# Performance work log

Measured on AMD Instinct MI355X. Metric: run time of the kernel, lower is better.

Reference implementation:

```python
import jax, jax.numpy as jnp
import numpy as np

DEPTH = 8
INPUT_WIDTH = 64
INNER_WIDTH = 32
BATCH = 65536
N_NODES = 2 ** DEPTH - 1   # 255 inner nodes
N_LEAVES = 2 ** DEPTH      # 256 bins
EPS = 1e-8


def _tree_paths(depth):
    """For each leaf, the inner-node index at each level and whether the path
    goes right (right child uses 1 - decision, mirroring hstack([p, 1-p]) indexing)."""
    node_idx = np.zeros((2 ** depth, depth), dtype=np.int32)
    is_right = np.zeros((2 ** depth, depth), dtype=bool)
    for leaf in range(2 ** depth):
        idx = 0
        for level in range(depth):
            bit = (leaf >> (depth - 1 - level)) & 1
            node_idx[leaf, level] = idx
            is_right[leaf, level] = bool(bit)
            idx = 2 * idx + 1 + bit
    return node_idx, is_right

_NODE_IDX_NP, _IS_RIGHT_NP = _tree_paths(DEPTH)
NODE_IDX = jnp.asarray(_NODE_IDX_NP)   # [L, depth]
IS_RIGHT = jnp.asarray(_IS_RIGHT_NP)   # [L, depth]


def _init_b_i():
    """Replicates PartialRadialLayer.init_tree_weights: thresholds evenly dividing [0,1],
    stored as logits so sigmoid(b_i) recovers the threshold."""
    b = np.zeros(N_NODES, dtype=np.float64)
    b[0] = -0.5
    used = 1
    for i in range(1, DEPTH):
        n_nodes = 2 ** i
        div = float(2 ** (i + 1))
        for node in range(n_nodes):
            b[used + node] = -(2 * node + 1) / div
        used += n_nodes
    return np.log(-b / (1.0 + b)).astype(np.float32).reshape(1, -1)


def setup_inputs() -> dict:
    key = jax.random.key(0)
    kx, kr, kt = jax.random.split(key, 3)
    x = jax.random.normal(kx, (BATCH, INPUT_WIDTH), dtype=jnp.float32)
    # kaiming_normal_ on [1, input_width]: fan_in = input_width
    ray = jax.random.normal(kr, (1, INPUT_WIDTH), dtype=jnp.float32) * np.sqrt(2.0 / INPUT_WIDTH)
    # kaiming_normal_ on [L, I, W]: fan_in = I * W
    inner_transforms = jax.random.normal(kt, (N_LEAVES, INPUT_WIDTH, INNER_WIDTH), dtype=jnp.float32) * np.sqrt(2.0 / (INPUT_WIDTH * INNER_WIDTH))
    w_i = jnp.zeros((1, N_NODES), dtype=jnp.float32)
    a_i = 5.0 * jnp.ones((1, N_NODES), dtype=jnp.float32)
    b_i = jnp.asarray(_init_b_i())
    return {"x": x, "ray": ray, "inner_transforms": inner_transforms,
            "w_i": w_i, "b_i": b_i, "a_i": a_i}


def reference(x, ray, inner_transforms, w_i, b_i, a_i):
    # angles: arccos(cosine_similarity(x, ray)) / pi
    x_norm = jnp.maximum(jnp.linalg.norm(x, axis=1), EPS)            # [B]
    r_norm = jnp.maximum(jnp.linalg.norm(ray, axis=1), EPS)          # [1]
    cos = jnp.clip((x @ ray[0]) / (x_norm * r_norm), -1.0, 1.0)      # [B]
    angles = jnp.arccos(cos) / jnp.pi                                # [B]

    # per-node decisions
    node_fns = (0.5 + jax.nn.sigmoid(w_i)) * angles[:, None] - jax.nn.sigmoid(b_i)  # [B, N]
    decisions = jax.nn.sigmoid(node_fns * (1.0 + a_i))                               # [B, N]

    # soft bin distribution: product along each root-to-leaf path
    g = decisions[:, NODE_IDX]                       # [B, L, depth]
    vals = jnp.where(IS_RIGHT, 1.0 - g, g)           # right child -> 1 - p
    distribution = jnp.prod(vals, axis=2)            # [B, L]

    # weighted per-leaf transforms: einsum('bi,liw->blw') then ('bl,blo->bo'), fused
    out = jnp.einsum('bl,bi,liw->bw', distribution, x, inner_transforms)
    return out
```

## Files before the change

### kernel.cpp

```cpp
#include <hip/hip_runtime.h>
#include <hip/hip_bf16.h>

#define NLEAF 256
#define MBLK 256
#define THREADS 512

typedef __attribute__((ext_vector_type(4))) float f32x4;
typedef __attribute__((ext_vector_type(4))) unsigned int uint4v;
typedef __attribute__((ext_vector_type(8))) __bf16 bf16x8;
typedef __attribute__((ext_vector_type(4))) __bf16 bf16x4;

#define OFF_DIST 0
#define OFF_XP   131072
#define OFF_AC   147456
#define OFF_BC   148480
#define OFF_ANG  149504
#define OFF_RAY  150528
#define SMEM_BYTES 150784

__device__ __forceinline__ float sigf(float s) { return 1.0f / (1.0f + __expf(-s)); }

__device__ __forceinline__ int permr(int r) {
  return (r & 0xC3) | ((r & 0x30) >> 2) | ((r & 0x0C) << 2);
}

__global__ __launch_bounds__(256) void prep_T(const float* __restrict__ T,
                                              __bf16* __restrict__ wsT) {
  __shared__ char tile[4096];
  const int l = blockIdx.x;
  const float* src = T + (size_t)l * 2048;
  const int t = threadIdx.x;
#pragma unroll
  for (int p = 0; p < 2; ++p) {
    int e = p * 1024 + t * 4;
    f32x4 v = *(const f32x4*)(src + e);
    int k = e >> 5, w0 = e & 31;
#pragma unroll
    for (int j = 0; j < 4; ++j) {
      int w = w0 + j;
      int off = (w * 128 + 2 * k) ^ ((w & 7) << 4);
      *(__bf16*)(tile + off) = (__bf16)v[j];
    }
  }
  __syncthreads();
  *(uint4v*)((char*)wsT + (size_t)l * 4096 + t * 16) = *(const uint4v*)(tile + t * 16);
}

template <bool USE_WS>
__global__ __launch_bounds__(THREADS, 2)
void prl_main(const float* __restrict__ x, const float* __restrict__ ray,
              const float* __restrict__ w_i, const float* __restrict__ b_i,
              const float* __restrict__ a_i, const void* __restrict__ tsrc,
              float* __restrict__ out) {
  extern __shared__ char smem[];
  const int tid = threadIdx.x;
  const int lane = tid & 63;
  const int wid = tid >> 6;
  const int rg = wid >> 1;
  const int cg = wid & 1;
  const int g = lane >> 4;
  const int ln = lane & 15;
  const int row0 = blockIdx.x * MBLK;

  float* A_c = (float*)(smem + OFF_AC);
  float* B_c = (float*)(smem + OFF_BC);
  float* angles = (float*)(smem + OFF_ANG);
  float* ray_l = (float*)(smem + OFF_RAY);
  __bf16* distb = (__bf16*)(smem + OFF_DIST);

  if (tid < 255) {
    float aa = 1.0f + a_i[tid];
    A_c[tid] = (0.5f + sigf(w_i[tid])) * aa;
    B_c[tid] = -sigf(b_i[tid]) * aa;
  }
  if (tid >= 256 && tid < 320) ray_l[tid - 256] = ray[tid - 256];
  __syncthreads();

  bf16x8 afrag[4][2] = {};
  float* xp = (float*)(smem + OFF_XP);
  for (int c = 0; c < 4; ++c) {
    const float* xg = x + (size_t)(row0 + c * 64) * 64;
#pragma unroll
    for (int p = 0; p < 2; ++p) {
      int idx = p * 512 + tid;
      f32x4 v = *(const f32x4*)(xg + idx * 4);
      *(f32x4*)(xp + idx * 4) = v;
      int cgr = idx & 15;
      f32x4 rv = *(const f32x4*)(ray_l + cgr * 4);
      float a0 = v[0] * v[0] + v[1] * v[1] + v[2] * v[2] + v[3] * v[3];
      float a1 = v[0] * rv[0] + v[1] * rv[1] + v[2] * rv[2] + v[3] * rv[3];
      float a2 = rv[0] * rv[0] + rv[1] * rv[1] + rv[2] * rv[2] + rv[3] * rv[3];
#pragma unroll
      for (int s = 1; s < 16; s <<= 1) {
        a0 += __shfl_xor(a0, s, 64);
        a1 += __shfl_xor(a1, s, 64);
        a2 += __shfl_xor(a2, s, 64);
      }
      if ((tid & 15) == 0) {
        int r = idx >> 4;
        float xn = fmaxf(sqrtf(a0), 1e-8f);
        float rn = fmaxf(sqrtf(a2), 1e-8f);
        float cs = a1 / (xn * rn);
        cs = fminf(fmaxf(cs, -1.0f), 1.0f);
        angles[c * 64 + r] = acosf(cs) * 0.31830988618379067f;
      }
    }
    __syncthreads();
    if (rg == c) {
#pragma unroll
      for (int mt = 0; mt < 4; ++mt)
#pragma unroll
        for (int kt = 0; kt < 2; ++kt) {
          int rl = mt * 16 + ln;
          int k0 = kt * 32 + g * 8;
          f32x4 u0 = *(const f32x4*)(xp + rl * 64 + k0);
          f32x4 u1 = *(const f32x4*)(xp + rl * 64 + k0 + 4);
          bf16x8 af;
          af[0] = (__bf16)u0[0]; af[1] = (__bf16)u0[1];
          af[2] = (__bf16)u0[2]; af[3] = (__bf16)u0[3];
          af[4] = (__bf16)u1[0]; af[5] = (__bf16)u1[1];
          af[6] = (__bf16)u1[2]; af[7] = (__bf16)u1[3];
          afrag[mt][kt] = af;
        }
    }
    __syncthreads();
  }

  __bf16* PA = (__bf16*)(smem + OFF_XP);
  __bf16* PB = (__bf16*)(smem + OFF_XP + 8192);
  if (tid < 256) {
    float ang = angles[tid];
    float d = sigf(fmaf(A_c[0], ang, B_c[0]));
    PA[tid] = (__bf16)d;
    PA[256 + tid] = (__bf16)(1.0f - d);
  }
  __syncthreads();
  {
    int n = tid >> 8, r = tid & 255;
    float p = (float)PA[tid];
    float ang = angles[r];
    float d = sigf(fmaf(A_c[1 + n], ang, B_c[1 + n]));
    PB[(2 * n) * 256 + r] = (__bf16)(p * d);
    PB[(2 * n + 1) * 256 + r] = (__bf16)(p * (1.0f - d));
  }
  __syncthreads();
#pragma unroll
  for (int it = 0; it < 2; ++it) {
    int e = it * 512 + tid;
    int n = e >> 8, r = e & 255;
    float p = (float)PB[e];
    float ang = angles[r];
    float d = sigf(fmaf(A_c[3 + n], ang, B_c[3 + n]));
    PA[(2 * n) * 256 + r] = (__bf16)(p * d);
    PA[(2 * n + 1) * 256 + r] = (__bf16)(p * (1.0f - d));
  }
  __syncthreads();
#pragma unroll
  for (int it = 0; it < 4; ++it) {
    int e = it * 512 + tid;
    int n = e >> 8, r = e & 255;
    float p = (float)PA[e];
    float ang = angles[r];
    float d = sigf(fmaf(A_c[7 + n], ang, B_c[7 + n]));
    PB[(2 * n) * 256 + r] = (__bf16)(p * d);
    PB[(2 * n + 1) * 256 + r] = (__bf16)(p * (1.0f - d));
  }
  __syncthreads();
  {
    const int r = tid & 255;
    const int pr = permr(r);
    const float ang = angles[r];
#pragma unroll
    for (int it = 0; it < 8; ++it) {
      int n4 = it * 2 + (tid >> 8);
      float p4 = (float)PB[n4 * 256 + r];
      float d4 = sigf(fmaf(A_c[15 + n4], ang, B_c[15 + n4]));
      float p5[2] = {p4 * d4, p4 * (1.0f - d4)};
#pragma unroll
      for (int b5 = 0; b5 < 2; ++b5) {
        int n5 = 2 * n4 + b5;
        float d5 = sigf(fmaf(A_c[31 + n5], ang, B_c[31 + n5]));
        float p6[2] = {p5[b5] * d5, p5[b5] * (1.0f - d5)};
#pragma unroll
        for (int b6 = 0; b6 < 2; ++b6) {
          int n6 = 2 * n5 + b6;
          float d6 = sigf(fmaf(A_c[63 + n6], ang, B_c[63 + n6]));
          float p7[2] = {p6[b6] * d6, p6[b6] * (1.0f - d6)};
#pragma unroll
          for (int b7 = 0; b7 < 2; ++b7) {
            int n7 = 2 * n6 + b7;
            float d7 = sigf(fmaf(A_c[127 + n7], ang, B_c[127 + n7]));
            float pv = p7[b7];
            distb[(2 * n7) * 256 + pr] = (__bf16)(pv * d7);
            distb[(2 * n7 + 1) * 256 + pr] = (__bf16)(pv * (1.0f - d7));
          }
        }
      }
    }
  }
  __syncthreads();

  f32x4 acc[4] = {};
  const int wB = cg * 16 + ln;
  const int ad0 = (wB * 128 + g * 16) ^ ((wB & 7) << 4);
  const int ad1 = (wB * 128 + 64 + g * 16) ^ ((wB & 7) << 4);

  auto compute = [&](bf16x8 bk0, bf16x8 bk1, int l) {
    const __bf16* dp = distb + l * 256 + rg * 64 + g * 16;
    bf16x8 q0 = *(const bf16x8*)dp;
    bf16x8 q1 = *(const bf16x8*)(dp + 8);
    f32x4 dv[4];
    dv[0] = (f32x4){(float)q0[0], (float)q0[1], (float)q0[2], (float)q0[3]};
    dv[1] = (f32x4){(float)q0[4], (float)q0[5], (float)q0[6], (float)q0[7]};
    dv[2] = (f32x4){(float)q1[0], (float)q1[1], (float)q1[2], (float)q1[3]};
    dv[3] = (f32x4){(float)q1[4], (float)q1[5], (float)q1[6], (float)q1[7]};
    f32x4 zero = {0.0f, 0.0f, 0.0f, 0.0f};
#pragma unroll
    for (int mt = 0; mt < 4; ++mt) {
      f32x4 y = __builtin_amdgcn_mfma_f32_16x16x32_bf16(afrag[mt][0], bk0, zero, 0, 0, 0);
      y = __builtin_amdgcn_mfma_f32_16x16x32_bf16(afrag[mt][1], bk1, y, 0, 0, 0);
      acc[mt] += dv[mt] * y;
    }
  };

  char* tb = smem + OFF_XP;

  if constexpr (USE_WS) {
    const int ts = tid >> 8;
    const int to = (tid & 255) * 16;
    uint4v tv = *(const uint4v*)((const char*)tsrc + ts * 4096 + to);
    *(uint4v*)(tb + ts * 4096 + to) = tv;
    tv = *(const uint4v*)((const char*)tsrc + (2 + ts) * 4096 + to);
    __syncthreads();
    for (int l = 0; l < NLEAF; l += 2) {
      char* cur = tb + ((l >> 1) & 1) * 8192;
      char* nxt = tb + (((l >> 1) + 1) & 1) * 8192;
      if (l + 2 < NLEAF) {
        *(uint4v*)(nxt + ts * 4096 + to) = tv;
        if (l + 4 < NLEAF)
          tv = *(const uint4v*)((const char*)tsrc + (size_t)(l + 4 + ts) * 4096 + to);
      }
      compute(*(const bf16x8*)(cur + ad0), *(const bf16x8*)(cur + ad1), l);
      compute(*(const bf16x8*)(cur + 4096 + ad0), *(const bf16x8*)(cur + 4096 + ad1), l + 1);
      __syncthreads();
    }
  } else {
    for (int l = 0; l < NLEAF; ++l) {
      const float* tp0 = (const float*)tsrc + (size_t)l * 2048 + (g * 8) * 32 + wB;
      const float* tp1 = tp0 + 32 * 32;
      bf16x8 bk0, bk1;
#pragma unroll
      for (int j = 0; j < 8; ++j) {
        bk0[j] = (__bf16)tp0[j * 32];
        bk1[j] = (__bf16)tp1[j * 32];
      }
      compute(bk0, bk1, l);
    }
  }

#pragma unroll
  for (int mt = 0; mt < 4; ++mt)
#pragma unroll
    for (int e = 0; e < 4; ++e) {
      int row = row0 + rg * 64 + mt * 16 + g * 4 + e;
      out[(size_t)row * 32 + cg * 16 + ln] = acc[mt][e];
    }
}

extern "C" void kernel_launch(void* const* d_in, const int* in_sizes, int n_in,
                              void* d_out, int out_size, void* d_ws, size_t ws_size,
                              hipStream_t stream) {
  const float* x = (const float*)d_in[0];
  const float* ray = (const float*)d_in[1];
  const float* T = (const float*)d_in[2];
  const float* w_i = (const float*)d_in[3];
  const float* b_i = (const float*)d_in[4];
  const float* a_i = (const float*)d_in[5];
  float* out = (float*)d_out;

  bool use_ws = ws_size >= (size_t)NLEAF * 4096;
  if (use_ws) {
    hipFuncSetAttribute(reinterpret_cast<const void*>(&prl_main<true>),
                        hipFuncAttributeMaxDynamicSharedMemorySize, SMEM_BYTES);
    prep_T<<<256, 256, 0, stream>>>(T, (__bf16*)d_ws);
    prl_main<true><<<256, THREADS, SMEM_BYTES, stream>>>(x, ray, w_i, b_i, a_i, d_ws, out);
  } else {
    hipFuncSetAttribute(reinterpret_cast<const void*>(&prl_main<false>),
                        hipFuncAttributeMaxDynamicSharedMemorySize, SMEM_BYTES);
    prl_main<false><<<256, THREADS, SMEM_BYTES, stream>>>(x, ray, w_i, b_i, a_i, T, out);
  }
}
```

Baseline: 174.6 us.

## Halve rows per block to double grid size and fit more blocks per CU

Each block now handles 128 rows instead of 256, so the grid has 512 blocks instead of 256. Shared memory is roughly halved and the launch bound now asks for 4 blocks per SM, both aimed at raising occupancy and filling all CUs. The leaf loop now stages one leaf of the transform per iteration instead of two, which means a barrier on every leaf. Each block also reloads the full bf16 transform set, so total transform traffic from L2 doubles.

Result: faster. 165.3 us (-5.3%).

```diff
diff --git a/kernel.cpp b/kernel.cpp
--- a/kernel.cpp
+++ b/kernel.cpp
@@ -2,7 +2,7 @@
 #include <hip/hip_bf16.h>
 
 #define NLEAF 256
-#define MBLK 256
+#define MBLK 128
 #define THREADS 512
 
 typedef __attribute__((ext_vector_type(4))) float f32x4;
@@ -11,17 +11,17 @@
 typedef __attribute__((ext_vector_type(4))) __bf16 bf16x4;
 
 #define OFF_DIST 0
-#define OFF_XP   131072
-#define OFF_AC   147456
-#define OFF_BC   148480
-#define OFF_ANG  149504
-#define OFF_RAY  150528
-#define SMEM_BYTES 150784
+#define OFF_T    65536
+#define OFF_AC   73728
+#define OFF_BC   74752
+#define OFF_ANG  75776
+#define OFF_RAY  76288
+#define SMEM_BYTES 76544
 
 __device__ __forceinline__ float sigf(float s) { return 1.0f / (1.0f + __expf(-s)); }
 
 __device__ __forceinline__ int permr(int r) {
-  return (r & 0xC3) | ((r & 0x30) >> 2) | ((r & 0x0C) << 2);
+  return (r & 0x63) | ((r & 0x0C) << 1) | ((r & 0x10) >> 2);
 }
 
 __global__ __launch_bounds__(256) void prep_T(const float* __restrict__ T,
@@ -47,7 +47,7 @@
 }
 
 template <bool USE_WS>
-__global__ __launch_bounds__(THREADS, 2)
+__global__ __launch_bounds__(THREADS, 4)
 void prl_main(const float* __restrict__ x, const float* __restrict__ ray,
               const float* __restrict__ w_i, const float* __restrict__ b_i,
               const float* __restrict__ a_i, const void* __restrict__ tsrc,
@@ -76,12 +76,11 @@
   if (tid >= 256 && tid < 320) ray_l[tid - 256] = ray[tid - 256];
   __syncthreads();
 
-  bf16x8 afrag[4][2] = {};
-  float* xp = (float*)(smem + OFF_XP);
-  for (int c = 0; c < 4; ++c) {
-    const float* xg = x + (size_t)(row0 + c * 64) * 64;
-#pragma unroll
-    for (int p = 0; p < 2; ++p) {
+  float* xp = (float*)(smem + OFF_DIST);
+  {
+    const float* xg = x + (size_t)row0 * 64;
+#pragma unroll
+    for (int p = 0; p < 4; ++p) {
       int idx = p * 512 + tid;
       f32x4 v = *(const f32x4*)(xg + idx * 4);
       *(f32x4*)(xp + idx * 4) = v;
@@ -102,78 +101,76 @@
         float rn = fmaxf(sqrtf(a2), 1e-8f);
         float cs = a1 / (xn * rn);
         cs = fminf(fmaxf(cs, -1.0f), 1.0f);
-        angles[c * 64 + r] = acosf(cs) * 0.31830988618379067f;
-      }
-    }
-    __syncthreads();
-    if (rg == c) {
-#pragma unroll
-      for (int mt = 0; mt < 4; ++mt)
-#pragma unroll
-        for (int kt = 0; kt < 2; ++kt) {
-          int rl = mt * 16 + ln;
-          int k0 = kt * 32 + g * 8;
-          f32x4 u0 = *(const f32x4*)(xp + rl * 64 + k0);
-          f32x4 u1 = *(const f32x4*)(xp + rl * 64 + k0 + 4);
-          bf16x8 af;
-          af[0] = (__bf16)u0[0]; af[1] = (__bf16)u0[1];
-          af[2] = (__bf16)u0[2]; af[3] = (__bf16)u0[3];
-          af[4] = (__bf16)u1[0]; af[5] = (__bf16)u1[1];
-          af[6] = (__bf16)u1[2]; af[7] = (__bf16)u1[3];
-          afrag[mt][kt] = af;
-        }
-    }
-    __syncthreads();
-  }
-
-  __bf16* PA = (__bf16*)(smem + OFF_XP);
-  __bf16* PB = (__bf16*)(smem + OFF_XP + 8192);
-  if (tid < 256) {
+        angles[r] = acosf(cs) * 0.31830988618379067f;
+      }
+    }
+  }
+  __syncthreads();
+
+  bf16x8 afrag[2][2];
+#pragma unroll
+  for (int mt = 0; mt < 2; ++mt)
+#pragma unroll
+    for (int kt = 0; kt < 2; ++kt) {
+      int rl = rg * 32 + mt * 16 + ln;
+      int k0 = kt * 32 + g * 8;
+      f32x4 u0 = *(const f32x4*)(xp + rl * 64 + k0);
+      f32x4 u1 = *(const f32x4*)(xp + rl * 64 + k0 + 4);
+      bf16x8 af;
+      af[0] = (__bf16)u0[0]; af[1] = (__bf16)u0[1];
+      af[2] = (__bf16)u0[2]; af[3] = (__bf16)u0[3];
+      af[4] = (__bf16)u1[0]; af[5] = (__bf16)u1[1];
+      af[6] = (__bf16)u1[2]; af[7] = (__bf16)u1[3];
+      afrag[mt][kt] = af;
+    }
+  __syncthreads();
+
+  __bf16* PA = (__bf16*)(smem + OFF_T);
+  __bf16* PB = (__bf16*)(smem + OFF_T + 4096);
+  if (tid < 128) {
     float ang = angles[tid];
     float d = sigf(fmaf(A_c[0], ang, B_c[0]));
     PA[tid] = (__bf16)d;
-    PA[256 + tid] = (__bf16)(1.0f - d);
-  }
-  __syncthreads();
-  {
-    int n = tid >> 8, r = tid & 255;
+    PA[128 + tid] = (__bf16)(1.0f - d);
+  }
+  __syncthreads();
+  if (tid < 256) {
+    int n = tid >> 7, r = tid & 127;
     float p = (float)PA[tid];
     float ang = angles[r];
     float d = sigf(fmaf(A_c[1 + n], ang, B_c[1 + n]));
-    PB[(2 * n) * 256 + r] = (__bf16)(p * d);
-    PB[(2 * n + 1) * 256 + r] = (__bf16)(p * (1.0f - d));
+    PB[(2 * n) * 128 + r] = (__bf16)(p * d);
+    PB[(2 * n + 1) * 128 + r] = (__bf16)(p * (1.0f - d));
+  }
+  __syncthreads();
+  {
+    int n = tid >> 7, r = tid & 127;
+    float p = (float)PB[tid];
+    float ang = angles[r];
+    float d = sigf(fmaf(A_c[3 + n], ang, B_c[3 + n]));
+    PA[(2 * n) * 128 + r] = (__bf16)(p * d);
+    PA[(2 * n + 1) * 128 + r] = (__bf16)(p * (1.0f - d));
   }
   __syncthreads();
 #pragma unroll
   for (int it = 0; it < 2; ++it) {
     int e = it * 512 + tid;
-    int n = e >> 8, r = e & 255;
-    float p = (float)PB[e];
-    float ang = angles[r];
-    float d = sigf(fmaf(A_c[3 + n], ang, B_c[3 + n]));
-    PA[(2 * n) * 256 + r] = (__bf16)(p * d);
-    PA[(2 * n + 1) * 256 + r] = (__bf16)(p * (1.0f - d));
-  }
-  __syncthreads();
-#pragma unroll
-  for (int it = 0; it < 4; ++it) {
-    int e = it * 512 + tid;
-    int n = e >> 8, r = e & 255;
+    int n = e >> 7, r = e & 127;
     float p = (float)PA[e];
     float ang = angles[r];
     float d = sigf(fmaf(A_c[7 + n], ang, B_c[7 + n]));
-    PB[(2 * n) * 256 + r] = (__bf16)(p * d);
-    PB[(2 * n + 1) * 256 + r] = (__bf16)(p * (1.0f - d));
+    PB[(2 * n) * 128 + r] = (__bf16)(p * d);
+    PB[(2 * n + 1) * 128 + r] = (__bf16)(p * (1.0f - d));
   }
   __syncthreads();
   {
-    const int r = tid & 255;
+    const int r = tid & 127;
     const int pr = permr(r);
     const float ang = angles[r];
 #pragma unroll
-    for (int it = 0; it < 8; ++it) {
-      int n4 = it * 2 + (tid >> 8);
-      float p4 = (float)PB[n4 * 256 + r];
+    for (int it = 0; it < 4; ++it) {
+      int n4 = it * 4 + (tid >> 7);
+      float p4 = (float)PB[n4 * 128 + r];
       float d4 = sigf(fmaf(A_c[15 + n4], ang, B_c[15 + n4]));
       float p5[2] = {p4 * d4, p4 * (1.0f - d4)};
 #pragma unroll
@@ -191,80 +188,77 @@
             int n7 = 2 * n6 + b7;
             float d7 = sigf(fmaf(A_c[127 + n7], ang, B_c[127 + n7]));
             float pv = p7[b7];
-            distb[(2 * n7) * 256 + pr] = (__bf16)(pv * d7);
-            distb[(2 * n7 + 1) * 256 + pr] = (__bf16)(pv * (1.0f - d7));
+            distb[(2 * n7) * 128 + pr] = (__bf16)(pv * d7);
+            distb[(2 * n7 + 1) * 128 + pr] = (__bf16)(pv * (1.0f - d7));
           }
         }
       }
     }
   }
-  __syncthreads();
-
-  f32x4 acc[4] = {};
+
+  f32x4 acc0 = {}, acc1 = {};
   const int wB = cg * 16 + ln;
   const int ad0 = (wB * 128 + g * 16) ^ ((wB & 7) << 4);
   const int ad1 = (wB * 128 + 64 + g * 16) ^ ((wB & 7) << 4);
-
-  auto compute = [&](bf16x8 bk0, bf16x8 bk1, int l) {
-    const __bf16* dp = distb + l * 256 + rg * 64 + g * 16;
-    bf16x8 q0 = *(const bf16x8*)dp;
-    bf16x8 q1 = *(const bf16x8*)(dp + 8);
-    f32x4 dv[4];
-    dv[0] = (f32x4){(float)q0[0], (float)q0[1], (float)q0[2], (float)q0[3]};
-    dv[1] = (f32x4){(float)q0[4], (float)q0[5], (float)q0[6], (float)q0[7]};
-    dv[2] = (f32x4){(float)q1[0], (float)q1[1], (float)q1[2], (float)q1[3]};
-    dv[3] = (f32x4){(float)q1[4], (float)q1[5], (float)q1[6], (float)q1[7]};
-    f32x4 zero = {0.0f, 0.0f, 0.0f, 0.0f};
-#pragma unroll
-    for (int mt = 0; mt < 4; ++mt) {
-      f32x4 y = __builtin_amdgcn_mfma_f32_16x16x32_bf16(afrag[mt][0], bk0, zero, 0, 0, 0);
-      y = __builtin_amdgcn_mfma_f32_16x16x32_bf16(afrag[mt][1], bk1, y, 0, 0, 0);
-      acc[mt] += dv[mt] * y;
-    }
-  };
-
-  char* tb = smem + OFF_XP;
-
+  char* tb = smem + OFF_T;
+
+  uint4v tv = {};
   if constexpr (USE_WS) {
-    const int ts = tid >> 8;
-    const int to = (tid & 255) * 16;
-    uint4v tv = *(const uint4v*)((const char*)tsrc + ts * 4096 + to);
-    *(uint4v*)(tb + ts * 4096 + to) = tv;
-    tv = *(const uint4v*)((const char*)tsrc + (2 + ts) * 4096 + to);
-    __syncthreads();
-    for (int l = 0; l < NLEAF; l += 2) {
-      char* cur = tb + ((l >> 1) & 1) * 8192;
-      char* nxt = tb + (((l >> 1) + 1) & 1) * 8192;
-      if (l + 2 < NLEAF) {
-        *(uint4v*)(nxt + ts * 4096 + to) = tv;
-        if (l + 4 < NLEAF)
-          tv = *(const uint4v*)((const char*)tsrc + (size_t)(l + 4 + ts) * 4096 + to);
-      }
-      compute(*(const bf16x8*)(cur + ad0), *(const bf16x8*)(cur + ad1), l);
-      compute(*(const bf16x8*)(cur + 4096 + ad0), *(const bf16x8*)(cur + 4096 + ad1), l + 1);
-      __syncthreads();
-    }
-  } else {
-    for (int l = 0; l < NLEAF; ++l) {
+    if (tid < 256) {
+      tv = *(const uint4v*)((const char*)tsrc + tid * 16);
+    }
+  }
+  __syncthreads();
+  if constexpr (USE_WS) {
+    if (tid < 256) {
+      *(uint4v*)(tb + tid * 16) = tv;
+      tv = *(const uint4v*)((const char*)tsrc + 4096 + tid * 16);
+    }
+  }
+  __syncthreads();
+
+  const f32x4 zero = {0.0f, 0.0f, 0.0f, 0.0f};
+  for (int l = 0; l < NLEAF; ++l) {
+    char* cur = tb + (l & 1) * 4096;
+    char* nxt = tb + ((l + 1) & 1) * 4096;
+    if constexpr (USE_WS) {
+      if (tid < 256) {
+        if (l + 1 < NLEAF) *(uint4v*)(nxt + tid * 16) = tv;
+        if (l + 2 < NLEAF)
+          tv = *(const uint4v*)((const char*)tsrc + (size_t)(l + 2) * 4096 + tid * 16);
+      }
+    }
+    bf16x8 q = *(const bf16x8*)(distb + l * 128 + rg * 32 + g * 8);
+    f32x4 dv0 = (f32x4){(float)q[0], (float)q[1], (float)q[2], (float)q[3]};
+    f32x4 dv1 = (f32x4){(float)q[4], (float)q[5], (float)q[6], (float)q[7]};
+    bf16x8 b0, b1;
+    if constexpr (USE_WS) {
+      b0 = *(const bf16x8*)(cur + ad0);
+      b1 = *(const bf16x8*)(cur + ad1);
+    } else {
       const float* tp0 = (const float*)tsrc + (size_t)l * 2048 + (g * 8) * 32 + wB;
       const float* tp1 = tp0 + 32 * 32;
-      bf16x8 bk0, bk1;
 #pragma unroll
       for (int j = 0; j < 8; ++j) {
-        bk0[j] = (__bf16)tp0[j * 32];
-        bk1[j] = (__bf16)tp1[j * 32];
-      }
-      compute(bk0, bk1, l);
-    }
-  }
-
-#pragma unroll
-  for (int mt = 0; mt < 4; ++mt)
-#pragma unroll
-    for (int e = 0; e < 4; ++e) {
-      int row = row0 + rg * 64 + mt * 16 + g * 4 + e;
-      out[(size_t)row * 32 + cg * 16 + ln] = acc[mt][e];
-    }
+        b0[j] = (__bf16)tp0[j * 32];
+        b1[j] = (__bf16)tp1[j * 32];
+      }
+    }
+    f32x4 y0 = __builtin_amdgcn_mfma_f32_16x16x32_bf16(afrag[0][0], b0, zero, 0, 0, 0);
+    y0 = __builtin_amdgcn_mfma_f32_16x16x32_bf16(afrag[0][1], b1, y0, 0, 0, 0);
+    f32x4 y1 = __builtin_amdgcn_mfma_f32_16x16x32_bf16(afrag[1][0], b0, zero, 0, 0, 0);
+    y1 = __builtin_amdgcn_mfma_f32_16x16x32_bf16(afrag[1][1], b1, y1, 0, 0, 0);
+    acc0 += dv0 * y0;
+    acc1 += dv1 * y1;
+    if constexpr (USE_WS) __syncthreads();
+  }
+
+#pragma unroll
+  for (int e = 0; e < 4; ++e) {
+    int row = row0 + rg * 32 + g * 4 + e;
+    out[(size_t)row * 32 + cg * 16 + ln] = acc0[e];
+    out[(size_t)(row + 16) * 32 + cg * 16 + ln] = acc1[e];
+  }
 }
 
 extern "C" void kernel_launch(void* const* d_in, const int* in_sizes, int n_in,
@@ -278,15 +272,16 @@
   const float* a_i = (const float*)d_in[5];
   float* out = (float*)d_out;
 
+  const int nblk = 65536 / MBLK;
   bool use_ws = ws_size >= (size_t)NLEAF * 4096;
   if (use_ws) {
     hipFuncSetAttribute(reinterpret_cast<const void*>(&prl_main<true>),
                         hipFuncAttributeMaxDynamicSharedMemorySize, SMEM_BYTES);
     prep_T<<<256, 256, 0, stream>>>(T, (__bf16*)d_ws);
-    prl_main<true><<<256, THREADS, SMEM_BYTES, stream>>>(x, ray, w_i, b_i, a_i, d_ws, out);
+    prl_main<true><<<nblk, THREADS, SMEM_BYTES, stream>>>(x, ray, w_i, b_i, a_i, d_ws, out);
   } else {
     hipFuncSetAttribute(reinterpret_cast<const void*>(&prl_main<false>),
                         hipFuncAttributeMaxDynamicSharedMemorySize, SMEM_BYTES);
-    prl_main<false><<<256, THREADS, SMEM_BYTES, stream>>>(x, ray, w_i, b_i, a_i, T, out);
-  }
-}
+    prl_main<false><<<nblk, THREADS, SMEM_BYTES, stream>>>(x, ray, w_i, b_i, a_i, T, out);
+  }
+}
```
